# Kernel tuning notes

Measured on AMD Instinct MI355X. Metric: run time of the kernel, lower is better.

Reference implementation:

```python
import jax, jax.numpy as jnp
import numpy as np

HIDDEN = 1024
NUM_HEADS = 16
HEAD_DIM = HIDDEN // NUM_HEADS  # 64
WINDOW = 33
PAD = WINDOW // 2
B, S = 2, 2048


def setup_inputs() -> dict:
    key = jax.random.key(0)
    k = jax.random.split(key, 5)
    x = jax.random.normal(k[0], (B, S, HIDDEN), dtype=jnp.float32)
    w_qkv = jax.random.normal(k[1], (3 * HIDDEN, HIDDEN), dtype=jnp.float32) * 0.02
    b_qkv = jax.random.normal(k[2], (3 * HIDDEN,), dtype=jnp.float32) * 0.02
    w_out = jax.random.normal(k[3], (HIDDEN, HIDDEN), dtype=jnp.float32) * 0.02
    b_out = jax.random.normal(k[4], (HIDDEN,), dtype=jnp.float32) * 0.02
    return {"x": x, "w_qkv": w_qkv, "b_qkv": b_qkv, "w_out": w_out, "b_out": b_out}


def reference(x, w_qkv, b_qkv, w_out, b_out):
    b, s, _ = x.shape
    # fused qkv projection: (B,S,3H)
    qkv = x @ w_qkv.T + b_qkv
    # (B, NH, S, 3*HD) then split into q,k,v -- matches torch reshape+chunk layout
    qkv = qkv.reshape(b, s, NUM_HEADS, 3 * HEAD_DIM).transpose(0, 2, 1, 3)
    q, k, v = jnp.split(qkv, 3, axis=-1)  # each (B, NH, S, HD)
    # zero-pad keys/values along sequence; NOTE: original does NOT mask the
    # padded positions -- zero keys yield score 0 and participate in softmax.
    k_pad = jnp.pad(k, ((0, 0), (0, 0), (PAD, PAD), (0, 0)))
    v_pad = jnp.pad(v, ((0, 0), (0, 0), (PAD, PAD), (0, 0)))
    # window gather indices: position i attends padded slots i..i+WINDOW-1
    idx = jnp.arange(s)[:, None] + jnp.arange(WINDOW)[None, :]  # (S, W)
    k_win = k_pad[:, :, idx, :]  # (B, NH, S, W, HD)
    v_win = v_pad[:, :, idx, :]  # (B, NH, S, W, HD)
    scores = jnp.einsum("bhsd,bhswd->bhsw", q, k_win) / jnp.sqrt(
        jnp.asarray(HEAD_DIM, dtype=q.dtype)
    )
    attn = jax.nn.softmax(scores, axis=-1)
    ctx = jnp.einsum("bhsw,bhswd->bhsd", attn, v_win)  # (B, NH, S, HD)
    ctx = ctx.transpose(0, 2, 1, 3).reshape(b, s, HIDDEN)
    return ctx @ w_out.T + b_out
```

## Files before the change

kernel.cpp:

```cpp
#include <hip/hip_runtime.h>
#include <stdint.h>

#define NHEADS 16
#define HDIM 64
#define WIN 33
#define BATCH 2
#define SEQ 2048
#define MROWS (BATCH*SEQ)
#define PARTSZ (BATCH*NHEADS*SEQ*HDIM)

using f32x4 = __attribute__((ext_vector_type(4))) float;
using bf16x8 = __attribute__((ext_vector_type(8))) short;

__device__ inline short f2bf(float f) {
    union { float f; uint32_t u; } c; c.f = f;
    uint32_t u = c.u;
    uint32_t r = (u + 0x7fffu + ((u >> 16) & 1u)) >> 16;
    return (short)(uint16_t)r;
}

#define GLL16(g, l) __builtin_amdgcn_global_load_lds( \
        (const __attribute__((address_space(1))) void*)(g), \
        (__attribute__((address_space(3))) void*)(l), 16, 0, 0)
#define WAITV(n)  asm volatile("s_waitcnt vmcnt(" #n ")" ::: "memory")
#define WAITL0()  asm volatile("s_waitcnt lgkmcnt(0)" ::: "memory")
#define SBAR()    __builtin_amdgcn_s_barrier()
#define SCHED0()  __builtin_amdgcn_sched_barrier(0)

__global__ __launch_bounds__(256)
void cvt3_k(const float* __restrict__ x,  short* __restrict__ xb,
            const float* __restrict__ w1, short* __restrict__ w1b,
            const float* __restrict__ w2, short* __restrict__ w2b)
{
    const int i = blockIdx.x * 256 + threadIdx.x;
    const float* src; short* dstp; int off;
    if (i < 524288)      { src = x;  dstp = xb;  off = i; }
    else if (i < 917504) { src = w1; dstp = w1b; off = i - 524288; }
    else                 { src = w2; dstp = w2b; off = i - 917504; }
    const f32x4 v0 = *(const f32x4*)(src + (size_t)off * 8);
    const f32x4 v1 = *(const f32x4*)(src + (size_t)off * 8 + 4);
    bf16x8 o;
    o[0] = f2bf(v0[0]); o[1] = f2bf(v0[1]); o[2] = f2bf(v0[2]); o[3] = f2bf(v0[3]);
    o[4] = f2bf(v1[0]); o[5] = f2bf(v1[1]); o[6] = f2bf(v1[2]); o[7] = f2bf(v1[3]);
    *(bf16x8*)(dstp + (size_t)off * 8) = o;
}

__global__ __launch_bounds__(512, 2)
void gemm1_k(const short* __restrict__ A, const short* __restrict__ Bm,
             const float* __restrict__ bias, short* __restrict__ dst)
{
    __shared__ short As[2][16384];
    __shared__ short Bs[2][12288];
    const int tid  = threadIdx.x;
    const int lane = tid & 63;
    const int wv   = tid >> 6;
    const int wr = wv >> 2, wc = wv & 3;
    const int q15 = lane & 15, p = lane >> 4;

    int bid = blockIdx.x;
    bid = (bid & 7) * 32 + (bid >> 3);
    const int tmi = bid & 15, tni = bid >> 4;
    const int tm = tmi << 8;
    const int tn = tni * 192;

    const int ssl = (tid & 7) ^ ((tid >> 4) & 7);
    const short* Ag = A  + (size_t)(tm + (tid >> 3)) * 1024 + ssl * 8;
    const short* Bg = Bm + (size_t)(tn + (tid >> 3)) * 1024 + ssl * 8;

#define STGA(d, rowoff, koff) GLL16(Ag + (size_t)(rowoff) * 1024 + (koff), &As[d][(rowoff) * 64 + tid * 8])
#define STGB(d, rowoff, koff) GLL16(Bg + (size_t)(rowoff) * 1024 + (koff), &Bs[d][(rowoff) * 64 + tid * 8])
#define STAGE_A(d, koff) do { STGA(d,0,koff); STGA(d,64,koff); STGA(d,128,koff); STGA(d,192,koff); } while (0)
#define STAGE_B(d, koff) do { STGB(d,0,koff); STGB(d,64,koff); STGB(d,128,koff); } while (0)

    f32x4 acc[8][3];
#pragma unroll
    for (int mi = 0; mi < 8; ++mi)
#pragma unroll
        for (int ni = 0; ni < 3; ++ni) acc[mi][ni] = (f32x4)0.f;

    const int swz  = q15 >> 1;
    const int arow = (wr * 128 + q15) * 64;
    const int brow = (wc * 48 + q15) * 64;
    const int s0o  = (p ^ swz) * 8;
    const int s1o  = ((4 + p) ^ swz) * 8;

    STAGE_A(0, 0); STAGE_B(0, 0); STAGE_A(1, 64);
    WAITV(4); SBAR(); SCHED0();

    for (int kt = 0; kt < 16; ++kt) {
        const int d = kt & 1;
        const short* asd = &As[d][0];
        const short* bsd = &Bs[d][0];
        bf16x8 af[4][2], bf[2][2], bf2[2];

#pragma unroll
        for (int mi = 0; mi < 4; ++mi) {
            af[mi][0] = *(const bf16x8*)(asd + arow + mi * 1024 + s0o);
            af[mi][1] = *(const bf16x8*)(asd + arow + mi * 1024 + s1o);
        }
#pragma unroll
        for (int ni = 0; ni < 2; ++ni) {
            bf[ni][0] = *(const bf16x8*)(bsd + brow + ni * 1024 + s0o);
            bf[ni][1] = *(const bf16x8*)(bsd + brow + ni * 1024 + s1o);
        }
        if (kt < 15) STAGE_B(d ^ 1, (kt + 1) * 64);
        SBAR(); WAITL0(); SCHED0();
        __builtin_amdgcn_s_setprio(1);
#pragma unroll
        for (int mi = 0; mi < 4; ++mi)
#pragma unroll
            for (int ni = 0; ni < 2; ++ni) {
                acc[mi][ni] = __builtin_amdgcn_mfma_f32_16x16x32_bf16(af[mi][0], bf[ni][0], acc[mi][ni], 0, 0, 0);
                acc[mi][ni] = __builtin_amdgcn_mfma_f32_16x16x32_bf16(af[mi][1], bf[ni][1], acc[mi][ni], 0, 0, 0);
            }
        __builtin_amdgcn_s_setprio(0);
        SBAR(); SCHED0();

        bf2[0] = *(const bf16x8*)(bsd + brow + 2 * 1024 + s0o);
        bf2[1] = *(const bf16x8*)(bsd + brow + 2 * 1024 + s1o);
        SBAR(); WAITL0(); SCHED0();
        __builtin_amdgcn_s_setprio(1);
#pragma unroll
        for (int mi = 0; mi < 4; ++mi) {
            acc[mi][2] = __builtin_amdgcn_mfma_f32_16x16x32_bf16(af[mi][0], bf2[0], acc[mi][2], 0, 0, 0);
            acc[mi][2] = __builtin_amdgcn_mfma_f32_16x16x32_bf16(af[mi][1], bf2[1], acc[mi][2], 0, 0, 0);
        }
        __builtin_amdgcn_s_setprio(0);
        SBAR(); SCHED0();

#pragma unroll
        for (int mi = 0; mi < 4; ++mi) {
            af[mi][0] = *(const bf16x8*)(asd + arow + (mi + 4) * 1024 + s0o);
            af[mi][1] = *(const bf16x8*)(asd + arow + (mi + 4) * 1024 + s1o);
        }
        SBAR(); WAITL0(); SCHED0();
        __builtin_amdgcn_s_setprio(1);
#pragma unroll
        for (int mi = 0; mi < 4; ++mi)
#pragma unroll
            for (int ni = 0; ni < 2; ++ni) {
                acc[mi + 4][ni] = __builtin_amdgcn_mfma_f32_16x16x32_bf16(af[mi][0], bf[ni][0], acc[mi + 4][ni], 0, 0, 0);
                acc[mi + 4][ni] = __builtin_amdgcn_mfma_f32_16x16x32_bf16(af[mi][1], bf[ni][1], acc[mi + 4][ni], 0, 0, 0);
            }
        __builtin_amdgcn_s_setprio(0);
        SBAR(); SCHED0();

        if (kt < 14) { STAGE_A(d, (kt + 2) * 64); WAITV(4); }
        else if (kt == 14) { WAITV(0); }
        SBAR(); SCHED0();
        __builtin_amdgcn_s_setprio(1);
#pragma unroll
        for (int mi = 0; mi < 4; ++mi) {
            acc[mi + 4][2] = __builtin_amdgcn_mfma_f32_16x16x32_bf16(af[mi][0], bf2[0], acc[mi + 4][2], 0, 0, 0);
            acc[mi + 4][2] = __builtin_amdgcn_mfma_f32_16x16x32_bf16(af[mi][1], bf2[1], acc[mi + 4][2], 0, 0, 0);
        }
        __builtin_amdgcn_s_setprio(0);
        SBAR(); SCHED0();
    }
#undef STGA
#undef STGB
#undef STAGE_A
#undef STAGE_B

#pragma unroll
    for (int mi = 0; mi < 8; ++mi) {
#pragma unroll
        for (int ni = 0; ni < 3; ++ni) {
            const int c    = wc * 48 + ni * 16 + q15;
            const int part = c >> 6;
            const int dd   = c & 63;
            const int row0 = tm + wr * 128 + mi * 16 + p * 4;
            const float bv = bias[tn + c];
            const size_t pbase = (size_t)part * PARTSZ;
#pragma unroll
            for (int r = 0; r < 4; ++r) {
                const int row = row0 + r;
                const int b   = row >> 11;
                const int s   = row & 2047;
                const size_t hb = pbase + ((((size_t)b << 4) + tni) << 17);
                const size_t addr = (part == 2)
                    ? hb + ((size_t)dd << 11) + s
                    : hb + ((size_t)s << 6) + dd;
                dst[addr] = f2bf(acc[mi][ni][r] + bv);
            }
        }
    }
}

__global__ __launch_bounds__(256, 3)
void gemm2_k(const short* __restrict__ A, const short* __restrict__ Bm,
             const float* __restrict__ bias, float* __restrict__ C)
{
    __shared__ short As[3][2048];
    __shared__ short Bs[3][4096];
    const int tid  = threadIdx.x;
    const int lane = tid & 63;
    const int wc   = tid >> 6;
    const int q15 = lane & 15, p = lane >> 4;

    int bid = blockIdx.x;
    bid = (bid & 7) * 64 + (bid >> 3);
    const int tm = (bid & 63) << 6;
    const int tn = (bid >> 6) << 7;

    const int rb  = tid >> 2;
    const int ssl = (tid & 3) ^ ((rb >> 1) & 3);
    const short* Ag = A  + (size_t)(tm + rb) * 1024 + ssl * 8;
    const short* Bg = Bm + (size_t)(tn + rb) * 1024 + ssl * 8;

#define STAGE2(tt, db) do {                                  \
        const int _ko = (tt) * 32;                           \
        GLL16(Ag + _ko,         &As[db][tid * 8]);           \
        GLL16(Bg + _ko,         &Bs[db][tid * 8]);           \
        GLL16(Bg + _ko + 65536, &Bs[db][2048 + tid * 8]);    \
    } while (0)

    f32x4 acc[4][2];
#pragma unroll
    for (int mi = 0; mi < 4; ++mi)
#pragma unroll
        for (int ni = 0; ni < 2; ++ni) acc[mi][ni] = (f32x4)0.f;

    int oA[4], oB[2];
#pragma unroll
    for (int mi = 0; mi < 4; ++mi) {
        const int row = mi * 16 + q15;
        oA[mi] = row * 32 + (p ^ ((row >> 1) & 3)) * 8;
    }
#pragma unroll
    for (int ni = 0; ni < 2; ++ni) {
        const int row = wc * 32 + ni * 16 + q15;
        oB[ni] = row * 32 + (p ^ ((row >> 1) & 3)) * 8;
    }

    STAGE2(0, 0); STAGE2(1, 1);
    WAITV(3); SBAR(); SCHED0();

    for (int t = 0; t < 32; ++t) {
        const int cb = t % 3;
        if (t < 30) STAGE2(t + 2, (t + 2) % 3);
        bf16x8 af[4], bfr[2];
#pragma unroll
        for (int mi = 0; mi < 4; ++mi) af[mi] = *(const bf16x8*)(&As[cb][oA[mi]]);
#pragma unroll
        for (int ni = 0; ni < 2; ++ni) bfr[ni] = *(const bf16x8*)(&Bs[cb][oB[ni]]);
        __builtin_amdgcn_s_setprio(1);
#pragma unroll
        for (int mi = 0; mi < 4; ++mi)
#pragma unroll
            for (int ni = 0; ni < 2; ++ni)
                acc[mi][ni] = __builtin_amdgcn_mfma_f32_16x16x32_bf16(af[mi], bfr[ni], acc[mi][ni], 0, 0, 0);
        __builtin_amdgcn_s_setprio(0);
        SCHED0();
        if (t < 30)       { WAITV(3); SBAR(); SCHED0(); }
        else if (t == 30) { WAITV(0); SBAR(); SCHED0(); }
    }
#undef STAGE2

#pragma unroll
    for (int mi = 0; mi < 4; ++mi) {
#pragma unroll
        for (int ni = 0; ni < 2; ++ni) {
            const int col  = tn + wc * 32 + ni * 16 + q15;
            const int row0 = tm + mi * 16 + p * 4;
            const float bv = bias[col];
#pragma unroll
            for (int r = 0; r < 4; ++r)
                C[(size_t)(row0 + r) * 1024 + col] = acc[mi][ni][r] + bv;
        }
    }
}

__global__ __launch_bounds__(256)
void swattn4_k(const short* __restrict__ qkvb, short* __restrict__ ctx)
{
    __shared__ short Ks[96 * 64];
    __shared__ short Vt[64 * 104];
    const int tid  = threadIdx.x;
    const int lane = tid & 63;
    const int w    = tid >> 6;
    const int q15  = lane & 15;
    const int p    = lane >> 4;
    const int tile = blockIdx.x & 31;
    const int bh   = blockIdx.x >> 5;
    const int b    = bh >> 4, h = bh & 15;
    const int s0   = tile * 64;
    const short* qbase  = qkvb + ((size_t)bh << 17);
    const short* kbase  = qbase + PARTSZ;
    const short* vtbase = qbase + 2 * PARTSZ;

#pragma unroll
    for (int c = 0; c < 3; ++c) {
        const int idx = c * 256 + tid;
        const int row = idx >> 3;
        const int sli = idx & 7;
        const int pos = s0 - 16 + row;
        bf16x8 kv = (bf16x8)0;
        if (pos >= 0 && pos < SEQ)
            kv = *(const bf16x8*)(kbase + (size_t)pos * 64 + sli * 8);
        *(bf16x8*)(Ks + row * 64 + ((sli ^ (row & 7)) << 3)) = kv;
    }
#pragma unroll
    for (int c = 0; c < 4; ++c) {
        const int idx = c * 256 + tid;
        const int d   = idx >> 4;
        const int sli = idx & 15;
        if (sli < 12) {
            const int pos = s0 - 16 + sli * 8;
            bf16x8 vv = (bf16x8)0;
            if (pos >= 0 && pos <= SEQ - 8)
                vv = *(const bf16x8*)(vtbase + (size_t)d * SEQ + pos);
            *(bf16x8*)(Vt + d * 104 + sli * 8) = vv;
        }
    }
    __syncthreads();

    const int qrow = s0 + w * 16 + q15;
    const bf16x8 qf0 = *(const bf16x8*)(qbase + (size_t)qrow * 64 + p * 8);
    const bf16x8 qf1 = *(const bf16x8*)(qbase + (size_t)qrow * 64 + 32 + p * 8);

    f32x4 accs[6];
#pragma unroll
    for (int t = 0; t < 6; ++t) accs[t] = (f32x4)0.f;
#pragma unroll
    for (int t = 0; t < 6; ++t) {
        const int row = t * 16 + q15;
        const int sw  = row & 7;
        const bf16x8 kf0 = *(const bf16x8*)(Ks + row * 64 + ((p ^ sw) << 3));
        const bf16x8 kf1 = *(const bf16x8*)(Ks + row * 64 + (((p + 4) ^ sw) << 3));
        accs[t] = __builtin_amdgcn_mfma_f32_16x16x32_bf16(kf0, qf0, accs[t], 0, 0, 0);
        accs[t] = __builtin_amdgcn_mfma_f32_16x16x32_bf16(kf1, qf1, accs[t], 0, 0, 0);
    }

    const int qloc = w * 16 + q15;
    float m = -1e30f;
#pragma unroll
    for (int t = 0; t < 6; ++t)
#pragma unroll
        for (int r = 0; r < 4; ++r) {
            const int n = t * 16 + p * 4 + r;
            const bool valid = (n >= qloc) && (n <= qloc + 32);
            const float v = valid ? accs[t][r] * 0.125f : -1e30f;
            accs[t][r] = v;
            m = fmaxf(m, v);
        }
    m = fmaxf(m, __shfl_xor(m, 16));
    m = fmaxf(m, __shfl_xor(m, 32));
    float sum = 0.f;
#pragma unroll
    for (int t = 0; t < 6; ++t)
#pragma unroll
        for (int r = 0; r < 4; ++r) {
            const float e = __expf(accs[t][r] - m);
            accs[t][r] = e;
            sum += e;
        }
    sum += __shfl_xor(sum, 16);
    sum += __shfl_xor(sum, 32);
    const float inv = 1.f / sum;

    uint32_t pk[6][2];
#pragma unroll
    for (int t = 0; t < 6; ++t)
#pragma unroll
        for (int rp = 0; rp < 2; ++rp) {
            const float lo = accs[t][2 * rp] * inv;
            const float hi = accs[t][2 * rp + 1] * inv;
            uint32_t o;
            asm("v_cvt_pk_bf16_f32 %0, %1, %2" : "=v"(o) : "v"(lo), "v"(hi));
            pk[t][rp] = o;
        }
    uint32_t afu[3][4];
#pragma unroll
    for (int t = 0; t < 6; ++t)
#pragma unroll
        for (int rp = 0; rp < 2; ++rp)
#pragma unroll
            for (int bb = 0; bb < 2; ++bb) {
                const int src = q15 + (((2 * p + bb) & 3) << 4);
                const uint32_t v = __shfl((int)pk[t][rp], src);
                if ((t & 1) == (p >> 1))
                    afu[t >> 1][2 * bb + rp] = v;
            }
    union U { uint32_t u[4]; bf16x8 v; };
    U u0, u1, u2;
#pragma unroll
    for (int f = 0; f < 4; ++f) { u0.u[f] = afu[0][f]; u1.u[f] = afu[1][f]; u2.u[f] = afu[2][f]; }
    const bf16x8 af0 = u0.v, af1 = u1.v, af2 = u2.v;

    f32x4 accp[4];
#pragma unroll
    for (int dt = 0; dt < 4; ++dt) accp[dt] = (f32x4)0.f;
#pragma unroll
    for (int dt = 0; dt < 4; ++dt) {
        const short* vr = Vt + (dt * 16 + q15) * 104 + p * 8;
        const bf16x8 vf0 = *(const bf16x8*)(vr);
        const bf16x8 vf1 = *(const bf16x8*)(vr + 32);
        const bf16x8 vf2 = *(const bf16x8*)(vr + 64);
        accp[dt] = __builtin_amdgcn_mfma_f32_16x16x32_bf16(af0, vf0, accp[dt], 0, 0, 0);
        accp[dt] = __builtin_amdgcn_mfma_f32_16x16x32_bf16(af1, vf1, accp[dt], 0, 0, 0);
        accp[dt] = __builtin_amdgcn_mfma_f32_16x16x32_bf16(af2, vf2, accp[dt], 0, 0, 0);
    }

#pragma unroll
    for (int dt = 0; dt < 4; ++dt) {
        const int d = dt * 16 + q15;
#pragma unroll
        for (int r = 0; r < 4; ++r) {
            const int s = s0 + w * 16 + p * 4 + r;
            ctx[(((size_t)(b * SEQ + s)) << 10) + h * 64 + d] = f2bf(accp[dt][r]);
        }
    }
}

extern "C" void kernel_launch(void* const* d_in, const int* in_sizes, int n_in,
                              void* d_out, int out_size, void* d_ws, size_t ws_size,
                              hipStream_t stream)
{
    const float* x     = (const float*)d_in[0];
    const float* w_qkv = (const float*)d_in[1];
    const float* b_qkv = (const float*)d_in[2];
    const float* w_out = (const float*)d_in[3];
    const float* b_out = (const float*)d_in[4];
    float* out = (float*)d_out;

    char* ws = (char*)d_ws;
    short* x_bf    = (short*)(ws);
    short* wqkv_bf = (short*)(ws + (8ull  << 20));
    short* wout_bf = (short*)(ws + (14ull << 20));
    short* qkvb    = (short*)(ws + (16ull << 20));
    short* ctx     = (short*)(ws + (48ull << 20));

    cvt3_k<<<dim3(4096), 256, 0, stream>>>(x, x_bf, w_qkv, wqkv_bf, w_out, wout_bf);

    gemm1_k<<<dim3(256), 512, 0, stream>>>(x_bf, wqkv_bf, b_qkv, qkvb);

    swattn4_k<<<dim3((SEQ / 64) * BATCH * NHEADS), 256, 0, stream>>>(qkvb, (short*)ctx);

    gemm2_k<<<dim3(512), 256, 0, stream>>>(ctx, wout_bf, b_out, out);
}
```

Before: 82.16 us.

## Load GEMM1 B operand directly from global into registers, bypassing LDS

The QKV projection GEMM no longer stages weight tiles through shared memory. Each wave loads its B fragments straight from global memory into a double-buffered register array one k-step ahead, so the A-only LDS pipeline needs fewer barriers per iteration. This cuts LDS footprint and traffic but raises register pressure, and B is now read redundantly by the waves that share columns, adding global/L2 load volume and exposing load latency more directly.

```diff
diff --git a/kernel.cpp b/kernel.cpp
--- a/kernel.cpp
+++ b/kernel.cpp
@@ -50,7 +50,6 @@
              const float* __restrict__ bias, short* __restrict__ dst)
 {
     __shared__ short As[2][16384];
-    __shared__ short Bs[2][12288];
     const int tid  = threadIdx.x;
     const int lane = tid & 63;
     const int wv   = tid >> 6;
@@ -64,13 +63,17 @@
     const int tn = tni * 192;
 
     const int ssl = (tid & 7) ^ ((tid >> 4) & 7);
-    const short* Ag = A  + (size_t)(tm + (tid >> 3)) * 1024 + ssl * 8;
-    const short* Bg = Bm + (size_t)(tn + (tid >> 3)) * 1024 + ssl * 8;
+    const short* Ag = A + (size_t)(tm + (tid >> 3)) * 1024 + ssl * 8;
 
 #define STGA(d, rowoff, koff) GLL16(Ag + (size_t)(rowoff) * 1024 + (koff), &As[d][(rowoff) * 64 + tid * 8])
-#define STGB(d, rowoff, koff) GLL16(Bg + (size_t)(rowoff) * 1024 + (koff), &Bs[d][(rowoff) * 64 + tid * 8])
 #define STAGE_A(d, koff) do { STGA(d,0,koff); STGA(d,64,koff); STGA(d,128,koff); STGA(d,192,koff); } while (0)
-#define STAGE_B(d, koff) do { STGB(d,0,koff); STGB(d,64,koff); STGB(d,128,koff); } while (0)
+
+    const short* Bg0 = Bm + (size_t)(tn + wc * 48 + q15) * 1024 + p * 8;
+#define LOADB(par, kk) do {                                                   \
+        _Pragma("unroll") for (int ni = 0; ni < 3; ++ni)                      \
+        _Pragma("unroll") for (int ks = 0; ks < 2; ++ks)                      \
+            bfr[par][ni][ks] = *(const bf16x8*)(Bg0 + ni * 16384 + (kk) * 64 + ks * 32); \
+    } while (0)
 
     f32x4 acc[8][3];
 #pragma unroll
@@ -80,87 +83,67 @@
 
     const int swz  = q15 >> 1;
     const int arow = (wr * 128 + q15) * 64;
-    const int brow = (wc * 48 + q15) * 64;
     const int s0o  = (p ^ swz) * 8;
     const int s1o  = ((4 + p) ^ swz) * 8;
 
-    STAGE_A(0, 0); STAGE_B(0, 0); STAGE_A(1, 64);
-    WAITV(4); SBAR(); SCHED0();
-
+    bf16x8 bfr[2][3][2];
+
+    STAGE_A(0, 0);
+    LOADB(0, 0);
+    STAGE_A(1, 64);
+    LOADB(1, 1);
+    WAITV(10); SBAR(); SCHED0();
+
+#pragma unroll
     for (int kt = 0; kt < 16; ++kt) {
-        const int d = kt & 1;
-        const short* asd = &As[d][0];
-        const short* bsd = &Bs[d][0];
-        bf16x8 af[4][2], bf[2][2], bf2[2];
+        const int par = kt & 1;
+        const short* asd = &As[par][0];
+        bf16x8 af[4][2];
 
 #pragma unroll
         for (int mi = 0; mi < 4; ++mi) {
             af[mi][0] = *(const bf16x8*)(asd + arow + mi * 1024 + s0o);
             af[mi][1] = *(const bf16x8*)(asd + arow + mi * 1024 + s1o);
         }
-#pragma unroll
-        for (int ni = 0; ni < 2; ++ni) {
-            bf[ni][0] = *(const bf16x8*)(bsd + brow + ni * 1024 + s0o);
-            bf[ni][1] = *(const bf16x8*)(bsd + brow + ni * 1024 + s1o);
-        }
-        if (kt < 15) STAGE_B(d ^ 1, (kt + 1) * 64);
-        SBAR(); WAITL0(); SCHED0();
+        WAITL0(); SCHED0();
         __builtin_amdgcn_s_setprio(1);
 #pragma unroll
         for (int mi = 0; mi < 4; ++mi)
 #pragma unroll
-            for (int ni = 0; ni < 2; ++ni) {
-                acc[mi][ni] = __builtin_amdgcn_mfma_f32_16x16x32_bf16(af[mi][0], bf[ni][0], acc[mi][ni], 0, 0, 0);
-                acc[mi][ni] = __builtin_amdgcn_mfma_f32_16x16x32_bf16(af[mi][1], bf[ni][1], acc[mi][ni], 0, 0, 0);
+            for (int ni = 0; ni < 3; ++ni) {
+                acc[mi][ni] = __builtin_amdgcn_mfma_f32_16x16x32_bf16(af[mi][0], bfr[par][ni][0], acc[mi][ni], 0, 0, 0);
+                acc[mi][ni] = __builtin_amdgcn_mfma_f32_16x16x32_bf16(af[mi][1], bfr[par][ni][1], acc[mi][ni], 0, 0, 0);
             }
         __builtin_amdgcn_s_setprio(0);
-        SBAR(); SCHED0();
-
-        bf2[0] = *(const bf16x8*)(bsd + brow + 2 * 1024 + s0o);
-        bf2[1] = *(const bf16x8*)(bsd + brow + 2 * 1024 + s1o);
-        SBAR(); WAITL0(); SCHED0();
-        __builtin_amdgcn_s_setprio(1);
-#pragma unroll
-        for (int mi = 0; mi < 4; ++mi) {
-            acc[mi][2] = __builtin_amdgcn_mfma_f32_16x16x32_bf16(af[mi][0], bf2[0], acc[mi][2], 0, 0, 0);
-            acc[mi][2] = __builtin_amdgcn_mfma_f32_16x16x32_bf16(af[mi][1], bf2[1], acc[mi][2], 0, 0, 0);
-        }
-        __builtin_amdgcn_s_setprio(0);
-        SBAR(); SCHED0();
+        SCHED0();
 
 #pragma unroll
         for (int mi = 0; mi < 4; ++mi) {
             af[mi][0] = *(const bf16x8*)(asd + arow + (mi + 4) * 1024 + s0o);
             af[mi][1] = *(const bf16x8*)(asd + arow + (mi + 4) * 1024 + s1o);
         }
-        SBAR(); WAITL0(); SCHED0();
+        WAITL0(); SBAR(); SCHED0();
+        if (kt < 14) STAGE_A(par, (kt + 2) * 64);
         __builtin_amdgcn_s_setprio(1);
 #pragma unroll
         for (int mi = 0; mi < 4; ++mi)
 #pragma unroll
-            for (int ni = 0; ni < 2; ++ni) {
-                acc[mi + 4][ni] = __builtin_amdgcn_mfma_f32_16x16x32_bf16(af[mi][0], bf[ni][0], acc[mi + 4][ni], 0, 0, 0);
-                acc[mi + 4][ni] = __builtin_amdgcn_mfma_f32_16x16x32_bf16(af[mi][1], bf[ni][1], acc[mi + 4][ni], 0, 0, 0);
+            for (int ni = 0; ni < 3; ++ni) {
+                acc[mi + 4][ni] = __builtin_amdgcn_mfma_f32_16x16x32_bf16(af[mi][0], bfr[par][ni][0], acc[mi + 4][ni], 0, 0, 0);
+                acc[mi + 4][ni] = __builtin_amdgcn_mfma_f32_16x16x32_bf16(af[mi][1], bfr[par][ni][1], acc[mi + 4][ni], 0, 0, 0);
             }
         __builtin_amdgcn_s_setprio(0);
-        SBAR(); SCHED0();
-
-        if (kt < 14) { STAGE_A(d, (kt + 2) * 64); WAITV(4); }
-        else if (kt == 14) { WAITV(0); }
-        SBAR(); SCHED0();
-        __builtin_amdgcn_s_setprio(1);
-#pragma unroll
-        for (int mi = 0; mi < 4; ++mi) {
-            acc[mi + 4][2] = __builtin_amdgcn_mfma_f32_16x16x32_bf16(af[mi][0], bf2[0], acc[mi + 4][2], 0, 0, 0);
-            acc[mi + 4][2] = __builtin_amdgcn_mfma_f32_16x16x32_bf16(af[mi][1], bf2[1], acc[mi + 4][2], 0, 0, 0);
-        }
-        __builtin_amdgcn_s_setprio(0);
-        SBAR(); SCHED0();
+        SCHED0();
+        if (kt < 14) {
+            LOADB(par, kt + 2);
+            WAITV(10); SBAR(); SCHED0();
+        } else if (kt == 14) {
+            WAITV(0); SBAR(); SCHED0();
+        }
     }
 #undef STGA
-#undef STGB
 #undef STAGE_A
-#undef STAGE_B
+#undef LOADB
 
 #pragma unroll
     for (int mi = 0; mi < 8; ++mi) {
```

Result: slower. 88.96 us (+8.3%).
